# Kernel tuning notes

Hardware: AMD Instinct MI355X
Metric: run time of the kernel (lower is better)

## Reference

```python
import jax, jax.numpy as jnp
import numpy as np

B, S, H, NH = 2, 2048, 2048, 16
HD = H // NH


def setup_inputs() -> dict:
    key = jax.random.key(0)
    k1, k2, k3 = jax.random.split(key, 3)
    hidden_states = jax.random.normal(k1, (B, S, H), dtype=jnp.float32)
    # multiplicative causal mask [1,1,S,S] of 0/1 floats
    mask = jnp.tril(jnp.ones((S, S), dtype=jnp.float32))[None, None]
    w_qkv = jax.random.normal(k2, (3 * H, H), dtype=jnp.float32) * 0.02
    b_qkv = jnp.zeros((3 * H,), dtype=jnp.float32)
    w_o = jax.random.normal(k3, (H, H), dtype=jnp.float32) * 0.02
    b_o = jnp.zeros((H,), dtype=jnp.float32)
    return {"hidden_states": hidden_states, "mask": mask,
            "w_qkv": w_qkv, "b_qkv": b_qkv, "w_o": w_o, "b_o": b_o}


def reference(hidden_states, mask, w_qkv, b_qkv, w_o, b_o):
    b, s, h = hidden_states.shape
    # QKV projection (torch Linear: x @ W.T + b)
    qkv = jnp.einsum('bsh,oh->bso', hidden_states, w_qkv) + b_qkv
    q, k, v = jnp.split(qkv, 3, axis=-1)

    def heads(t):  # [b,s,nh*hd] -> [b,nh,s,hd]
        return t.reshape(b, s, NH, HD).transpose(0, 2, 1, 3)

    q, k, v = heads(q), heads(k), heads(v)
    q = q / jnp.sqrt(jnp.float32(HD)).astype(q.dtype)
    scores = jnp.einsum('bhqd,bhkd->bhqk', q, k)  # [b,nh,s,s]
    # custom multiplicative mask + -10000 bias
    scores = scores * mask - 10000.0 * (1.0 - mask)
    probs = jax.nn.softmax(scores, axis=-1)
    ctx = jnp.einsum('bhqk,bhkd->bhqd', probs, v)
    ctx = ctx.transpose(0, 2, 1, 3).reshape(b, s, h)  # [b,s,H]
    out = jnp.einsum('bsh,oh->bso', ctx, w_o) + b_o
    return out
```

## Files before the change

kernel.cpp:

```cpp
#include <hip/hip_runtime.h>


typedef _Float16 half_t;
typedef _Float16 f16x8 __attribute__((ext_vector_type(8)));
typedef _Float16 f16x4 __attribute__((ext_vector_type(4)));
typedef float f32x4 __attribute__((ext_vector_type(4)));

#define AS3(p) ((__attribute__((address_space(3))) void*)(p))
#define AS1(p) ((const __attribute__((address_space(1))) void*)(p))

constexpr int B_ = 2, S_ = 2048, H_ = 2048, NH_ = 16, HD_ = 128;
constexpr int M_ = B_ * S_;
constexpr int NQKV_ = 3 * H_;

union U2H4 { uint2 u; f16x4 h; };
union U4H8 { uint4 u; f16x8 h; };

__global__ void f32_to_f16_kernel(const float* __restrict__ src,
                                  half_t* __restrict__ dst, int n4) {
  int i = blockIdx.x * blockDim.x + threadIdx.x;
  int stride = gridDim.x * blockDim.x;
  for (; i < n4; i += stride) {
    float4 f = reinterpret_cast<const float4*>(src)[i];
    f16x4 h;
    h[0] = (half_t)f.x; h[1] = (half_t)f.y; h[2] = (half_t)f.z; h[3] = (half_t)f.w;
    reinterpret_cast<f16x4*>(dst)[i] = h;
  }
}

template <int EPI, int GX, int GY>
__global__ __launch_bounds__(256, 2) void gemm_nt(
    const half_t* __restrict__ A, const half_t* __restrict__ Bw,
    const float* __restrict__ bias,
    half_t* __restrict__ qp, half_t* __restrict__ kp, half_t* __restrict__ vp,
    float* __restrict__ outp) {
  constexpr int K_ = 2048;
  constexpr int NWG = GX * GY;
  static_assert(NWG % 8 == 0, "bijective chunked swizzle needs nwg%8==0");
  __shared__ __align__(16) half_t As[128 * 64];
  __shared__ __align__(16) half_t Bs[128 * 64];
  const int tid = threadIdx.x;
  const int lane = tid & 63;
  const int w = tid >> 6;
  const int wr = w >> 1, wc = w & 1;
  const int l15 = lane & 15, lg = lane >> 4;
  const int h = blockIdx.x;
  const int orig = (h & 7) * (NWG / 8) + (h >> 3);
  const int rowBase = (orig / GX) * 128;
  const int colBase = (orig % GX) * 128;

  f32x4 acc[4][4];
#pragma unroll
  for (int m = 0; m < 4; ++m)
#pragma unroll
    for (int n = 0; n < 4; ++n) acc[m][n] = {0.f, 0.f, 0.f, 0.f};

  for (int k0 = 0; k0 < K_; k0 += 64) {
#pragma unroll
    for (int pass = 0; pass < 4; ++pass) {
      int p = pass * 4096 + tid * 16;
      int row = p >> 7;
      int q = (p & 127) ^ ((row & 7) << 4);
      const half_t* ga = &A[(size_t)(rowBase + row) * K_ + k0 + (q >> 1)];
      __builtin_amdgcn_global_load_lds(AS1(ga), AS3((char*)As + (p & ~1023)), 16, 0, 0);
      const half_t* gb = &Bw[(size_t)(colBase + row) * K_ + k0 + (q >> 1)];
      __builtin_amdgcn_global_load_lds(AS1(gb), AS3((char*)Bs + (p & ~1023)), 16, 0, 0);
    }
    __syncthreads();
#pragma unroll
    for (int kk = 0; kk < 2; ++kk) {
      f16x8 af[4], bf[4];
#pragma unroll
      for (int m = 0; m < 4; ++m) {
        int row = wr * 64 + m * 16 + l15;
        int byte = row * 128 + ((kk * 64 + lg * 16) ^ ((row & 7) << 4));
        af[m] = *reinterpret_cast<const f16x8*>((const char*)As + byte);
      }
#pragma unroll
      for (int n = 0; n < 4; ++n) {
        int row = wc * 64 + n * 16 + l15;
        int byte = row * 128 + ((kk * 64 + lg * 16) ^ ((row & 7) << 4));
        bf[n] = *reinterpret_cast<const f16x8*>((const char*)Bs + byte);
      }
#pragma unroll
      for (int m = 0; m < 4; ++m)
#pragma unroll
        for (int n = 0; n < 4; ++n)
          acc[m][n] = __builtin_amdgcn_mfma_f32_16x16x32_f16(af[m], bf[n], acc[m][n], 0, 0, 0);
    }
    __syncthreads();
  }

#pragma unroll
  for (int m = 0; m < 4; ++m) {
    int trow = rowBase + wr * 64 + m * 16 + lg * 4;
#pragma unroll
    for (int n = 0; n < 4; ++n) {
      int col = colBase + wc * 64 + n * 16 + l15;
      float bv = bias[col];
      if constexpr (EPI == 0) {
        int which = col >> 11;
        int rem = col & 2047;
        int head = rem >> 7;
        int d = rem & 127;
        float scl = (which == 0) ? 0.08838834764831845f : 1.0f;
#pragma unroll
        for (int r = 0; r < 4; ++r) {
          int t = trow + r;
          int b = t >> 11, s = t & 2047;
          float v = (acc[m][n][r] + bv) * scl;
          if (which == 2) {
            vp[((size_t)((b * NH_ + head) * HD_ + d)) * S_ + s] = (half_t)v;
          } else {
            half_t* dst = (which == 0) ? qp : kp;
            dst[((size_t)((b * NH_ + head) * S_ + s)) * HD_ + d] = (half_t)v;
          }
        }
      } else {
#pragma unroll
        for (int r = 0; r < 4; ++r) {
          int t = trow + r;
          outp[(size_t)t * H_ + col] = acc[m][n][r] + bv;
        }
      }
    }
  }
}

__global__ __launch_bounds__(256, 4) void attn_kernel(
    const half_t* __restrict__ qp, const half_t* __restrict__ kp,
    const half_t* __restrict__ vtp, half_t* __restrict__ ctx) {
  __shared__ __align__(16) half_t Ks[64 * 128];
  __shared__ __align__(16) half_t Vt[128 * 64];

  const int tid = threadIdx.x;
  const int lane = tid & 63;
  const int w = tid >> 6;
  const int l15 = lane & 15, lg = lane >> 4;
  const int bh = blockIdx.y;
  const int qtile = (gridDim.x - 1) - blockIdx.x;
  const int q0 = qtile * 64;
  const int qw = q0 + w * 16;
  const int myq = qw + l15;

  f16x8 qf[4];
  {
    const half_t* qbase = qp + ((size_t)bh * S_ + myq) * HD_;
#pragma unroll
    for (int kk = 0; kk < 4; ++kk)
      qf[kk] = *reinterpret_cast<const f16x8*>(qbase + kk * 32 + lg * 8);
  }

  f32x4 oacc[8];
#pragma unroll
  for (int d = 0; d < 8; ++d) oacc[d] = {0.f, 0.f, 0.f, 0.f};
  float mrun = -1e30f, lrun = 0.f;

  const int nt = qtile + 1;
  for (int t = 0; t < nt; ++t) {
    const int k0 = t * 64;
    __syncthreads();
#pragma unroll
    for (int pass = 0; pass < 4; ++pass) {
      int p = pass * 4096 + tid * 16;
      int row = p >> 8;
      int q = (p & 255) ^ ((row & 7) << 4);
      const half_t* g = &kp[((size_t)bh * S_ + k0 + row) * HD_ + (q >> 1)];
      __builtin_amdgcn_global_load_lds(AS1(g), AS3((char*)Ks + (p & ~1023)), 16, 0, 0);
    }
#pragma unroll
    for (int pass = 0; pass < 4; ++pass) {
      int p = pass * 4096 + tid * 16;
      int row = p >> 7;
      int q = (p & 127) ^ ((row & 7) << 4);
      const half_t* g = &vtp[((size_t)bh * HD_ + row) * S_ + k0 + (q >> 1)];
      __builtin_amdgcn_global_load_lds(AS1(g), AS3((char*)Vt + (p & ~1023)), 16, 0, 0);
    }
    __syncthreads();

    f32x4 sc[4];
#pragma unroll
    for (int c = 0; c < 4; ++c) sc[c] = {0.f, 0.f, 0.f, 0.f};
#pragma unroll
    for (int kk = 0; kk < 4; ++kk) {
#pragma unroll
      for (int c = 0; c < 4; ++c) {
        int row = c * 16 + l15;
        int byte = row * 256 + ((kk * 64 + lg * 16) ^ ((row & 7) << 4));
        f16x8 kf = *reinterpret_cast<const f16x8*>((const char*)Ks + byte);
        sc[c] = __builtin_amdgcn_mfma_f32_16x16x32_f16(kf, qf[kk], sc[c], 0, 0, 0);
      }
    }

    float tm = -1e30f;
#pragma unroll
    for (int c = 0; c < 4; ++c) {
#pragma unroll
      for (int r = 0; r < 4; ++r) {
        int kg = k0 + c * 16 + lg * 4 + r;
        float s = (kg <= myq) ? sc[c][r] : -10000.0f;
        sc[c][r] = s;
        tm = fmaxf(tm, s);
      }
    }
    tm = fmaxf(tm, __shfl_xor(tm, 16));
    tm = fmaxf(tm, __shfl_xor(tm, 32));

    float mnew = fmaxf(mrun, tm);
    float alpha = __expf(mrun - mnew);
    mrun = mnew;
    float rs = 0.f;
#pragma unroll
    for (int c = 0; c < 4; ++c)
#pragma unroll
      for (int r = 0; r < 4; ++r) {
        float pv = __expf(sc[c][r] - mrun);
        sc[c][r] = pv;
        rs += pv;
      }
    rs += __shfl_xor(rs, 16);
    rs += __shfl_xor(rs, 32);
    lrun = lrun * alpha + rs;
#pragma unroll
    for (int d = 0; d < 8; ++d) oacc[d] *= alpha;

    uint2 pp[4];
#pragma unroll
    for (int c = 0; c < 4; ++c) {
      U2H4 u;
      u.h[0] = (half_t)sc[c][0]; u.h[1] = (half_t)sc[c][1];
      u.h[2] = (half_t)sc[c][2]; u.h[3] = (half_t)sc[c][3];
      pp[c] = u.u;
    }
    const int sA = (((2 * lg) & 3) << 4) + l15;
    const int sB = (((2 * lg + 1) & 3) << 4) + l15;
    const bool hi = (lg >= 2);
    f16x8 pf[2];
#pragma unroll
    for (int kk = 0; kk < 2; ++kk) {
      uint2 e = pp[2 * kk], o = pp[2 * kk + 1];
      uint2 ae, ao, be, bo;
      ae.x = __shfl((int)e.x, sA); ae.y = __shfl((int)e.y, sA);
      ao.x = __shfl((int)o.x, sA); ao.y = __shfl((int)o.y, sA);
      be.x = __shfl((int)e.x, sB); be.y = __shfl((int)e.y, sB);
      bo.x = __shfl((int)o.x, sB); bo.y = __shfl((int)o.y, sB);
      uint2 first = hi ? ao : ae;
      uint2 second = hi ? bo : be;
      U4H8 u; u.u = make_uint4(first.x, first.y, second.x, second.y);
      pf[kk] = u.h;
    }

#pragma unroll
    for (int dc = 0; dc < 8; ++dc) {
      int row = dc * 16 + l15;
#pragma unroll
      for (int kk = 0; kk < 2; ++kk) {
        int byte = row * 128 + ((kk * 64 + lg * 16) ^ ((row & 7) << 4));
        f16x8 vf = *reinterpret_cast<const f16x8*>((const char*)Vt + byte);
        oacc[dc] = __builtin_amdgcn_mfma_f32_16x16x32_f16(vf, pf[kk], oacc[dc], 0, 0, 0);
      }
    }
  }

  const int b = bh >> 4, h = bh & 15;
  const float rl = 1.0f / lrun;
  half_t* cbase = ctx + ((size_t)(b * S_ + myq)) * H_ + h * HD_;
#pragma unroll
  for (int dc = 0; dc < 8; ++dc) {
    U2H4 u;
    u.h[0] = (half_t)(oacc[dc][0] * rl);
    u.h[1] = (half_t)(oacc[dc][1] * rl);
    u.h[2] = (half_t)(oacc[dc][2] * rl);
    u.h[3] = (half_t)(oacc[dc][3] * rl);
    *reinterpret_cast<uint2*>(cbase + dc * 16 + lg * 4) = u.u;
  }
}

extern "C" void kernel_launch(void* const* d_in, const int* in_sizes, int n_in,
                              void* d_out, int out_size, void* d_ws, size_t ws_size,
                              hipStream_t stream) {
  (void)in_sizes; (void)n_in; (void)out_size; (void)ws_size;
  const float* hidden = (const float*)d_in[0];
  const float* w_qkv = (const float*)d_in[2];
  const float* b_qkv = (const float*)d_in[3];
  const float* w_o   = (const float*)d_in[4];
  const float* b_o   = (const float*)d_in[5];
  float* out = (float*)d_out;

  char* ws = (char*)d_ws;
  half_t* wqkvb = (half_t*)(ws + 0);
  half_t* wob   = (half_t*)(ws + 25165824);
  half_t* xb    = (half_t*)(ws + 33554432);
  half_t* qws   = (half_t*)(ws + 50331648);
  half_t* kws   = (half_t*)(ws + 67108864);
  half_t* vtws  = (half_t*)(ws + 83886080);
  half_t* ctx   = xb;

  f32_to_f16_kernel<<<2048, 256, 0, stream>>>(hidden, xb, M_ * H_ / 4);
  f32_to_f16_kernel<<<2048, 256, 0, stream>>>(w_qkv, wqkvb, NQKV_ * H_ / 4);
  f32_to_f16_kernel<<<2048, 256, 0, stream>>>(w_o, wob, H_ * H_ / 4);

  gemm_nt<0, NQKV_ / 128, M_ / 128><<<(NQKV_ / 128) * (M_ / 128), 256, 0, stream>>>(
      xb, wqkvb, b_qkv, qws, kws, vtws, nullptr);

  attn_kernel<<<dim3(S_ / 64, B_ * NH_), 256, 0, stream>>>(qws, kws, vtws, ctx);

  gemm_nt<1, H_ / 128, M_ / 128><<<(H_ / 128) * (M_ / 128), 256, 0, stream>>>(
      ctx, wob, b_o, nullptr, nullptr, nullptr, out);
}
```

Measured before the change: 457.2 us.

## Replace QKV GEMM with 256x256-tile, 8-wave, 4-deep pipelined LDS kernel

Adds a dedicated QKV projection kernel that uses 256x256 output tiles, 512 threads and a 4-stage ring of direct global-to-LDS loads with XOR swizzling. It interleaves staging with MFMA phases and raises wave priority during the matrix ops. The aim is to hide global memory latency and raise operand reuse per LDS load compared with the old 128x128 double-sync kernel. In exchange it uses 128 KB of LDS per block and 128 accumulator registers per lane, which limits occupancy, and 384 blocks may leave the tail unevenly balanced across CUs. The output-projection GEMM is simplified to its float-output epilogue only.

```diff
diff --git a/kernel.cpp b/kernel.cpp
--- a/kernel.cpp
+++ b/kernel.cpp
@@ -28,12 +28,122 @@
   }
 }
 
-template <int EPI, int GX, int GY>
+__global__ __launch_bounds__(512, 2) void gemm_qkv8(
+    const half_t* __restrict__ A, const half_t* __restrict__ Bw,
+    const float* __restrict__ bias,
+    half_t* __restrict__ qp, half_t* __restrict__ kp, half_t* __restrict__ vp) {
+  constexpr int K_ = 2048, GX = 24, NWG = 384, NT = 64;
+  __shared__ __align__(16) char lds[131072];
+  const int tid = threadIdx.x;
+  const int lane = tid & 63;
+  const int wid = tid >> 6;
+  const int wr = wid >> 2, wc = wid & 3;
+  const int l15 = lane & 15, lg = lane >> 4;
+  const int h = blockIdx.x;
+  const int orig = (h & 7) * (NWG / 8) + (h >> 3);
+  const int rowBase = (orig / GX) * 256;
+  const int colBase = (orig % GX) * 256;
+
+  f32x4 acc[8][4];
+#pragma unroll
+  for (int mf = 0; mf < 8; ++mf)
+#pragma unroll
+    for (int ni = 0; ni < 4; ++ni) acc[mf][ni] = {0.f, 0.f, 0.f, 0.f};
+
+  auto stage = [&](int ring, int mat, int k0) {
+#pragma unroll
+    for (int pass = 0; pass < 2; ++pass) {
+      int byte = pass * 8192 + tid * 16;
+      int row = byte >> 6;
+      int off = byte & 63;
+      int qs = off ^ (((row >> 1) & 3) << 4);
+      const half_t* g = mat
+          ? (Bw + (size_t)(colBase + row) * K_ + k0 + (qs >> 1))
+          : (A  + (size_t)(rowBase + row) * K_ + k0 + (qs >> 1));
+      __builtin_amdgcn_global_load_lds(
+          AS1(g), AS3(lds + ring * 32768 + mat * 16384 + byte), 16, 0, 0);
+    }
+  };
+
+#pragma unroll
+  for (int pt = 0; pt < 3; ++pt) { stage(pt, 0, pt * 32); stage(pt, 1, pt * 32); }
+  asm volatile("s_waitcnt vmcnt(8)" ::: "memory");
+  __builtin_amdgcn_s_barrier();
+
+  for (int t = 0; t < NT; ++t) {
+    const int ring = t & 3;
+    const int sring = (t + 3) & 3;
+    const int k0s = (t + 3) * 32;
+    const bool dostage = (t < NT - 3);
+#pragma unroll
+    for (int ph = 0; ph < 2; ++ph) {
+      f16x8 af[4], bf[4];
+#pragma unroll
+      for (int mi = 0; mi < 4; ++mi) {
+        int row = wr * 128 + (ph * 4 + mi) * 16 + l15;
+        af[mi] = *reinterpret_cast<const f16x8*>(
+            lds + ring * 32768 + row * 64 + ((lg * 16) ^ (((row >> 1) & 3) << 4)));
+      }
+#pragma unroll
+      for (int ni = 0; ni < 4; ++ni) {
+        int row = wc * 64 + ni * 16 + l15;
+        bf[ni] = *reinterpret_cast<const f16x8*>(
+            lds + ring * 32768 + 16384 + row * 64 + ((lg * 16) ^ (((row >> 1) & 3) << 4)));
+      }
+      if (dostage) stage(sring, ph, k0s);
+      __builtin_amdgcn_s_barrier();
+      asm volatile("s_waitcnt lgkmcnt(0)" ::: "memory");
+      __builtin_amdgcn_sched_barrier(0);
+      __builtin_amdgcn_s_setprio(1);
+#pragma unroll
+      for (int mi = 0; mi < 4; ++mi)
+#pragma unroll
+        for (int ni = 0; ni < 4; ++ni)
+          acc[ph * 4 + mi][ni] = __builtin_amdgcn_mfma_f32_16x16x32_f16(
+              af[mi], bf[ni], acc[ph * 4 + mi][ni], 0, 0, 0);
+      __builtin_amdgcn_s_setprio(0);
+      __builtin_amdgcn_sched_barrier(0);
+      if (ph == 1) {
+        if (t <= NT - 4)      asm volatile("s_waitcnt vmcnt(8)" ::: "memory");
+        else if (t == NT - 3) asm volatile("s_waitcnt vmcnt(4)" ::: "memory");
+        else if (t == NT - 2) asm volatile("s_waitcnt vmcnt(0)" ::: "memory");
+      }
+      __builtin_amdgcn_s_barrier();
+    }
+  }
+
+#pragma unroll
+  for (int mf = 0; mf < 8; ++mf) {
+    int trow = rowBase + wr * 128 + mf * 16 + lg * 4;
+#pragma unroll
+    for (int ni = 0; ni < 4; ++ni) {
+      int col = colBase + wc * 64 + ni * 16 + l15;
+      float bv = bias[col];
+      int which = col >> 11;
+      int rem = col & 2047;
+      int head = rem >> 7;
+      int d = rem & 127;
+      float scl = (which == 0) ? 0.08838834764831845f : 1.0f;
+#pragma unroll
+      for (int r = 0; r < 4; ++r) {
+        int tt = trow + r;
+        int b = tt >> 11, s = tt & 2047;
+        float v = (acc[mf][ni][r] + bv) * scl;
+        if (which == 2) {
+          vp[((size_t)((b * NH_ + head) * HD_ + d)) * S_ + s] = (half_t)v;
+        } else {
+          half_t* dst = (which == 0) ? qp : kp;
+          dst[((size_t)((b * NH_ + head) * S_ + s)) * HD_ + d] = (half_t)v;
+        }
+      }
+    }
+  }
+}
+
+template <int GX, int GY>
 __global__ __launch_bounds__(256, 2) void gemm_nt(
     const half_t* __restrict__ A, const half_t* __restrict__ Bw,
-    const float* __restrict__ bias,
-    half_t* __restrict__ qp, half_t* __restrict__ kp, half_t* __restrict__ vp,
-    float* __restrict__ outp) {
+    const float* __restrict__ bias, float* __restrict__ outp) {
   constexpr int K_ = 2048;
   constexpr int NWG = GX * GY;
   static_assert(NWG % 8 == 0, "bijective chunked swizzle needs nwg%8==0");
@@ -98,30 +208,10 @@
     for (int n = 0; n < 4; ++n) {
       int col = colBase + wc * 64 + n * 16 + l15;
       float bv = bias[col];
-      if constexpr (EPI == 0) {
-        int which = col >> 11;
-        int rem = col & 2047;
-        int head = rem >> 7;
-        int d = rem & 127;
-        float scl = (which == 0) ? 0.08838834764831845f : 1.0f;
-#pragma unroll
-        for (int r = 0; r < 4; ++r) {
-          int t = trow + r;
-          int b = t >> 11, s = t & 2047;
-          float v = (acc[m][n][r] + bv) * scl;
-          if (which == 2) {
-            vp[((size_t)((b * NH_ + head) * HD_ + d)) * S_ + s] = (half_t)v;
-          } else {
-            half_t* dst = (which == 0) ? qp : kp;
-            dst[((size_t)((b * NH_ + head) * S_ + s)) * HD_ + d] = (half_t)v;
-          }
-        }
-      } else {
-#pragma unroll
-        for (int r = 0; r < 4; ++r) {
-          int t = trow + r;
-          outp[(size_t)t * H_ + col] = acc[m][n][r] + bv;
-        }
+#pragma unroll
+      for (int r = 0; r < 4; ++r) {
+        int t = trow + r;
+        outp[(size_t)t * H_ + col] = acc[m][n][r] + bv;
       }
     }
   }
@@ -300,11 +390,10 @@
   f32_to_f16_kernel<<<2048, 256, 0, stream>>>(w_qkv, wqkvb, NQKV_ * H_ / 4);
   f32_to_f16_kernel<<<2048, 256, 0, stream>>>(w_o, wob, H_ * H_ / 4);
 
-  gemm_nt<0, NQKV_ / 128, M_ / 128><<<(NQKV_ / 128) * (M_ / 128), 256, 0, stream>>>(
-      xb, wqkvb, b_qkv, qws, kws, vtws, nullptr);
+  gemm_qkv8<<<384, 512, 0, stream>>>(xb, wqkvb, b_qkv, qws, kws, vtws);
 
   attn_kernel<<<dim3(S_ / 64, B_ * NH_), 256, 0, stream>>>(qws, kws, vtws, ctx);
 
-  gemm_nt<1, H_ / 128, M_ / 128><<<(H_ / 128) * (M_ / 128), 256, 0, stream>>>(
-      ctx, wob, b_o, nullptr, nullptr, nullptr, out);
-}
+  gemm_nt<H_ / 128, M_ / 128><<<(H_ / 128) * (M_ / 128), 256, 0, stream>>>(
+      ctx, wob, b_o, out);
+}
```

Result: slower. 468.0 us (+2.4%).
